# Optimization experiments

Measured on AMD Instinct MI355X. Metric: run time of the kernel, lower is better.

The kernel has to match this reference:

```python
import jax, jax.numpy as jnp
import numpy as np

R1, R2 = 0.1, 0.2  # initial_radius(0.0125) * 8, * 16
EPS = 1e-5

def sqdist(a, b):
    # a [B,N,3], b [B,M,3] -> [B,N,M]
    return jnp.sum(a * a, -1)[:, :, None] + jnp.sum(b * b, -1)[:, None, :] - 2.0 * jnp.einsum('bnc,bmc->bnm', a, b)

def gather(p, idx):
    # p [B,N,C], idx [B,...] -> [B,...,C]
    return jax.vmap(lambda pp, ii: pp[ii])(p, idx)

def fps(xyz, npoint):
    # farthest point sampling, returns int32 [B,npoint]
    B, N, _ = xyz.shape
    def step(carry, _):
        dist, far = carry
        cen = xyz[jnp.arange(B), far]                       # [B,3]
        d = jnp.sum((xyz - cen[:, None, :]) ** 2, -1)       # [B,N]
        dist = jnp.minimum(dist, d)
        nxt = jnp.argmax(dist, -1).astype(jnp.int32)
        return (dist, nxt), far
    init = (jnp.full((B, N), 1e10, xyz.dtype), jnp.zeros(B, jnp.int32))
    _, idx = jax.lax.scan(step, init, None, length=npoint)
    return idx.T

def ball_query(xyz, new_xyz, radius, nsample):
    d = sqdist(new_xyz, xyz)                                # [B,S,N]
    N = xyz.shape[1]
    cand = jnp.where(d <= radius * radius, jnp.arange(N, dtype=jnp.int32), jnp.int32(N))
    idx = -jax.lax.top_k(-cand, nsample)[0]                 # smallest nsample in-ball indices
    first = idx[..., :1]
    idx = jnp.where(idx == N, first, idx)                   # pad with first neighbor
    nearest = jnp.argmin(d, -1, keepdims=True).astype(jnp.int32)
    return jnp.where(idx == N, nearest, idx)                # fallback if ball empty

def bn_relu(x, g, b, axes):
    # training-mode batchnorm (biased var) + relu, channel-last
    m = jnp.mean(x, axes, keepdims=True)
    v = jnp.mean((x - m) ** 2, axes, keepdims=True)
    return jax.nn.relu((x - m) * jax.lax.rsqrt(v + EPS) * g + b)

def set_abstraction(xyz, feat, npoint, radius, nsample, layers):
    new_xyz = gather(xyz, fps(xyz, npoint))                 # [B,S,3]
    gidx = ball_query(xyz, new_xyz, radius, nsample)        # [B,S,K]
    gx = gather(xyz, gidx) - new_xyz[:, :, None, :]         # [B,S,K,3]
    h = jnp.concatenate([gx, gather(feat, gidx)], -1)       # [B,S,K,3+C]
    for w, g, b in layers:
        h = bn_relu(jnp.einsum('bskc,oc->bsko', h, w), g, b, (0, 1, 2))
    return new_xyz, jnp.max(h, 2)                           # [B,S,Cout]

def set_upconv(pos1, pos2, feat1, feat2, nsample, w1, g1, b1, w2, g2, b2):
    idx = jax.lax.top_k(-sqdist(pos1, pos2), nsample)[1]    # knn into sparse cloud [B,N,K]
    gp = gather(pos2, idx) - pos1[:, :, None, :]
    h = jnp.concatenate([gather(feat2, idx), gp], -1)       # [B,N,K,C2+3]
    h = bn_relu(jnp.einsum('bnkc,oc->bnko', h, w1), g1, b1, (0, 1, 2))
    h = jnp.max(h, 2)
    h = jnp.concatenate([h, feat1], -1)                     # [B,N,mlp[-1]+C1]
    return bn_relu(jnp.einsum('bnc,oc->bno', h, w2), g2, b2, (0, 1))

def feature_prop(pos1, pos2, feat1, feat2, w, g, b):
    negd, idx = jax.lax.top_k(-sqdist(pos1, pos2), 3)       # 3-NN
    dist = jnp.maximum(-negd, 1e-10)
    wgt = 1.0 / dist
    wgt = wgt / jnp.sum(wgt, -1, keepdims=True)
    interp = jnp.sum(gather(feat2, idx) * wgt[..., None], 2)
    h = jnp.concatenate([interp, feat1], -1)
    return bn_relu(jnp.einsum('bnc,oc->bno', h, w), g, b, (0, 1))

def _forward(points1, fea1, points2, fea2,
             sa1_w0, sa1_g0, sa1_b0, sa1_w1, sa1_g1, sa1_b1,
             sa2_w0, sa2_g0, sa2_b0, sa2_w1, sa2_g1, sa2_b1,
             su1_w1, su1_g1, su1_b1, su1_w2, su1_g2, su1_b2,
             fp_w, fp_g, fp_b, bn1_g, bn1_b, conv2_w, conv2_b):
    def pipeline(pts, fea):
        l1x, l1f = set_abstraction(pts, fea, 4096, R1, 16,
                                   [(sa1_w0, sa1_g0, sa1_b0), (sa1_w1, sa1_g1, sa1_b1)])
        l2x, l2f = set_abstraction(l1x, l1f, 1024, R2, 16,
                                   [(sa2_w0, sa2_g0, sa2_b0), (sa2_w1, sa2_g1, sa2_b1)])
        l1n = set_upconv(l1x, l2x, l1f, l2f, 8, su1_w1, su1_g1, su1_b1, su1_w2, su1_g2, su1_b2)
        l0n = feature_prop(pts, l1x, fea, l1n, fp_w, fp_g, fp_b)
        x = bn_relu(l0n, bn1_g, bn1_b, (0, 1))              # relu(bn1(.))
        sf = jnp.einsum('bnc,oc->bno', x, conv2_w) + conv2_b
        return jnp.concatenate([pts, sf], -1)               # include_pos
    return jnp.stack([pipeline(points1, fea1), pipeline(points2, fea2)])  # [2,B,N,19]

def setup_inputs() -> dict:
    key = jax.random.key(0)
    ks = jax.random.split(key, 12)
    B, N, C = 2, 8192, 10
    def w(k, o, i):
        return jax.random.normal(k, (o, i), jnp.float32) * 0.1
    inp = {
        'points1': jax.random.uniform(ks[0], (B, N, 3), jnp.float32),
        'fea1': jax.random.normal(ks[1], (B, N, C), jnp.float32),
        'points2': jax.random.uniform(ks[2], (B, N, 3), jnp.float32),
        'fea2': jax.random.normal(ks[3], (B, N, C), jnp.float32),
        'sa1_w0': w(ks[4], 16, 13), 'sa1_g0': jnp.ones(16), 'sa1_b0': jnp.zeros(16),
        'sa1_w1': w(ks[5], 32, 16), 'sa1_g1': jnp.ones(32), 'sa1_b1': jnp.zeros(32),
        'sa2_w0': w(ks[6], 32, 35), 'sa2_g0': jnp.ones(32), 'sa2_b0': jnp.zeros(32),
        'sa2_w1': w(ks[7], 64, 32), 'sa2_g1': jnp.ones(64), 'sa2_b1': jnp.zeros(64),
        'su1_w1': w(ks[8], 32, 67), 'su1_g1': jnp.ones(32), 'su1_b1': jnp.zeros(32),
        'su1_w2': w(ks[9], 32, 64), 'su1_g2': jnp.ones(32), 'su1_b2': jnp.zeros(32),
        'fp_w': w(ks[10], 32, 42), 'fp_g': jnp.ones(32), 'fp_b': jnp.zeros(32),
        'bn1_g': jnp.ones(32), 'bn1_b': jnp.zeros(32),
        'conv2_w': w(ks[11], 16, 32), 'conv2_b': jnp.zeros(16),
    }
    return inp

def reference(points1, fea1, points2, fea2,
              sa1_w0, sa1_g0, sa1_b0, sa1_w1, sa1_g1, sa1_b1,
              sa2_w0, sa2_g0, sa2_b0, sa2_w1, sa2_g1, sa2_b1,
              su1_w1, su1_g1, su1_b1, su1_w2, su1_g2, su1_b2,
              fp_w, fp_g, fp_b, bn1_g, bn1_b, conv2_w, conv2_b):
    return _forward(points1, fea1, points2, fea2,
                    sa1_w0, sa1_g0, sa1_b0, sa1_w1, sa1_g1, sa1_b1,
                    sa2_w0, sa2_g0, sa2_b0, sa2_w1, sa2_g1, sa2_b1,
                    su1_w1, su1_g1, su1_b1, su1_w2, su1_g2, su1_b2,
                    fp_w, fp_g, fp_b, bn1_g, bn1_b, conv2_w, conv2_b)
```

## Files before the change

### kernel.cpp

```cpp
#include <hip/hip_runtime.h>

#define DI __device__ __forceinline__

enum : int {
  OFF_XYZF = 0,
  OFF_FEAF = OFF_XYZF + 4*8192*3,
  OFF_NX1  = OFF_FEAF + 4*8192*10,
  OFF_L1F  = OFF_NX1  + 4*4096*3,
  OFF_NX2  = OFF_L1F  + 4*4096*32,
  OFF_L2F  = OFF_NX2  + 4*1024*3,
  OFF_UH2  = OFF_L2F  + 4*1024*64,
  OFF_L1N  = OFF_UH2  + 4*4096*32,
  OFF_H3   = OFF_L1N  + 4*4096*32,
  OFF_L0N  = OFF_H3   + 4*8192*32,
  OFF_STATS= OFF_L0N  + 4*8192*32,
  OFF_GIDX1= OFF_STATS + 2048,
  OFF_GIDX2= OFF_GIDX1 + 4*4096*16,
  OFF_UIDX = OFF_GIDX2 + 4*1024*16,
  WS_END   = OFF_UIDX + 4*4096*8
};
enum : int { ST_SA1A=0, ST_SA1B=64, ST_SA2A=128, ST_SA2B=192, ST_U1=320, ST_U2=384, ST_FP=448, ST_BN1=512 };

DI float nrm3(float x, float y, float z){ return fmaf(z,z, fmaf(y,y, x*x)); }
DI float dot3(float ax,float ay,float az,float bx,float by,float bz){
  return fmaf(az,bz, fmaf(ay,by, ax*bx));
}

template<int CTRL>
DI double kstage(double v){
  int lo = __builtin_amdgcn_update_dpp(0, __double2loint(v), CTRL, 0xf, 0xf, true);
  int hi = __builtin_amdgcn_update_dpp(0, __double2hiint(v), CTRL, 0xf, 0xf, true);
  return fmax(v, __hiloint2double(hi, lo));
}
DI double red63_kmax(double v){
  v = kstage<0x111>(v);
  v = kstage<0x112>(v);
  v = kstage<0x114>(v);
  v = kstage<0x118>(v);
  v = kstage<0x142>(v);
  v = kstage<0x143>(v);
  return v;
}

template<int CH>
DI void stats_accum(float* h, float* dst, float (*sred)[128])
{
  float sq[CH];
  #pragma unroll
  for (int c=0;c<CH;c++) sq[c]=h[c]*h[c];
  #pragma unroll
  for (int m=1;m<64;m<<=1){
    #pragma unroll
    for (int c=0;c<CH;c++){ h[c] += __shfl_xor(h[c], m, 64); sq[c] += __shfl_xor(sq[c], m, 64); }
  }
  const int tid=threadIdx.x, wid=tid>>6, lane=tid&63;
  if (lane==0){
    #pragma unroll
    for (int c=0;c<CH;c++){ sred[wid][c]=h[c]; sred[wid][CH+c]=sq[c]; }
  }
  __syncthreads();
  if (tid < 2*CH){
    float v = sred[0][tid]+sred[1][tid]+sred[2][tid]+sred[3][tid];
    atomicAdd(dst+tid, v);
  }
}

__global__ __launch_bounds__(256) void prep(const float* __restrict__ p1,const float* __restrict__ f1,
                                            const float* __restrict__ p2,const float* __restrict__ f2,
                                            float* __restrict__ xyzf, float* __restrict__ feaf)
{
  const int i = blockIdx.x*256+threadIdx.x;
  const int z = i>>13, n = i&8191, pipe=z>>1, b=z&1;
  const float* ps = (pipe?p2:p1) + (b*8192+n)*3;
  const float* fs = (pipe?f2:f1) + (b*8192+n)*10;
  float* xo = xyzf + (z*8192+n)*3;
  float* fo = feaf + (z*8192+n)*10;
  #pragma unroll
  for (int c=0;c<3;c++)  xo[c]=ps[c];
  #pragma unroll
  for (int c=0;c<10;c++) fo[c]=fs[c];
}

template<int N,int NPOINT,int T>
__global__ __launch_bounds__(T) void fps_kernel(const float* __restrict__ src, float* __restrict__ dst)
{
  constexpr int P = N/T;
  const int z = blockIdx.x;
  const float* xyz = src + z*N*3;
  float* nx = dst + z*NPOINT*3;
  const int t = threadIdx.x;
  __shared__ float sx[N], sy[N], szz[N];
  __shared__ int swin[NPOINT];
  __shared__ unsigned long long s_acc[3];
  float px[P],py[P],pz[P],dist[P];
  #pragma unroll
  for (int k=0;k<P;k++){
    const int j = t + k*T;
    float x=xyz[j*3+0], y=xyz[j*3+1], w=xyz[j*3+2];
    px[k]=x; py[k]=y; pz[k]=w; dist[k]=1e10f;
    sx[j]=x; sy[j]=y; szz[j]=w;
  }
  if (t==0){ s_acc[0]=0ull; s_acc[1]=0ull; s_acc[2]=0ull; }
  __syncthreads();
  unsigned long long win = (unsigned long long)(unsigned)(N-1);
  for (int s=0;;s++){
    const int cur = (N-1) - (int)(unsigned)(win & 0xffffffffull);
    if (t==0) swin[s] = cur;
    if (s == NPOINT-1) break;
    const float cx=sx[cur], cy=sy[cur], cz=szz[cur];
    float lm = -1.0f;
    #pragma unroll
    for (int k=0;k<P;k+=2){
      float dx0=px[k]-cx,   dy0=py[k]-cy,   dz0=pz[k]-cz;
      float dx1=px[k+1]-cx, dy1=py[k+1]-cy, dz1=pz[k+1]-cz;
      float d0 = fmaf(dz0,dz0, fmaf(dy0,dy0, dx0*dx0));
      float d1 = fmaf(dz1,dz1, fmaf(dy1,dy1, dx1*dx1));
      float n0 = fminf(dist[k],   d0);
      float n1 = fminf(dist[k+1], d1);
      dist[k]=n0; dist[k+1]=n1;
      lm = fmaxf(lm, fmaxf(n0,n1));
    }
    int kb = 0;
    #pragma unroll
    for (int k=P-1;k>=0;k--) if (dist[k]==lm) kb = k;
    double mykey = __hiloint2double(__float_as_int(lm), N-1 - (t + kb*T));
    double wk = red63_kmax(mykey);
    if ((t&63)==63)
      atomicMax(&s_acc[s%3], (unsigned long long)__double_as_longlong(wk));
    if (t==0) s_acc[(s+1)%3] = 0ull;
    __syncthreads();
    win = s_acc[s%3];
  }
  __syncthreads();
  for (int i=t;i<NPOINT;i+=T){
    int j = swin[i];
    nx[i*3]=sx[j]; nx[i*3+1]=sy[j]; nx[i*3+2]=szz[j];
  }
}

template<int NSRC,int SQ,int K>
__global__ __launch_bounds__(64) void ball_query(const float* __restrict__ qxyz, const float* __restrict__ sxyz,
                                                 int* __restrict__ gidx, float r2)
{
  __shared__ float4 tile[1024];
  const int z = blockIdx.y, tid = threadIdx.x;
  const int s = blockIdx.x*64 + tid;
  const float* q = qxyz + (z*SQ+s)*3;
  const float qx=q[0],qy=q[1],qz=q[2];
  const float qq=nrm3(qx,qy,qz);
  int cnt=0, first=0, amin=0; float dmin=3.0e38f;
  int* out = gidx + (z*SQ+s)*K;
  for (int t0=0;t0<NSRC;t0+=1024){
    __syncthreads();
    for (int i=tid;i<1024;i+=64){
      const float* p = sxyz + (z*NSRC+t0+i)*3;
      float x=p[0],y=p[1],w=p[2];
      tile[i]=make_float4(x,y,w,nrm3(x,y,w));
    }
    __syncthreads();
    for (int jj=0;jj<1024;jj++){
      float4 p = tile[jj];
      float dot=dot3(qx,qy,qz,p.x,p.y,p.z);
      float d=(qq+p.w)-2.0f*dot;
      const int j = t0+jj;
      if (d < dmin){ dmin=d; amin=j; }
      if (d <= r2 && cnt < K){ if(cnt==0) first=j; out[cnt]=j; cnt++; }
    }
  }
  const int fill = (cnt==0)? amin : first;
  for (int c=cnt;c<K;c++) out[c]=fill;
}

template<int S,int K,int CF,int C1,int C2,int NSRC,int PASS>
__global__ __launch_bounds__(256) void sa_pass(
    const float* __restrict__ srcxyz, const float* __restrict__ srcfea,
    const float* __restrict__ qxyz, const int* __restrict__ gidx,
    const float* __restrict__ w0, const float* __restrict__ g0, const float* __restrict__ b0,
    const float* __restrict__ w1, const float* __restrict__ g1v, const float* __restrict__ b1v,
    float* __restrict__ stats, int offA, int offB, float cnt0, float cnt1,
    float* __restrict__ outp)
{
  constexpr int CIN = 3+CF;
  __shared__ float w0l[C1*CIN];
  __shared__ float w1l[PASS>=2 ? C2*C1 : 1];
  __shared__ float sc0[C1], bi0[C1];
  __shared__ float sc1[C2], bi1[C2];
  __shared__ float sred[4][128];
  const int z = blockIdx.y, pipe = z>>1, tid = threadIdx.x;
  float* stA = stats + pipe*1024 + offA;
  float* stB = stats + pipe*1024 + offB;
  for (int i=tid;i<C1*CIN;i+=256) w0l[i]=w0[i];
  if (PASS>=2){
    for (int i=tid;i<C2*C1;i+=256) w1l[i]=w1[i];
    if (tid<C1){
      float m = stA[tid]/cnt0;
      float var = stA[C1+tid]/cnt0 - m*m;
      float rs = 1.0f/sqrtf(var+1e-5f);
      float sc = rs*g0[tid];
      sc0[tid]=sc; bi0[tid]=b0[tid]-m*sc;
    }
  }
  if (PASS==3 && tid<C2){
    float m = stB[tid]/cnt1;
    float var = stB[C2+tid]/cnt1 - m*m;
    float rs = 1.0f/sqrtf(var+1e-5f);
    float sc = rs*g1v[tid];
    sc1[tid]=sc; bi1[tid]=b1v[tid]-m*sc;
  }
  __syncthreads();
  const int item = blockIdx.x*256+tid;
  const int s = item/K;
  const int j = gidx[(z*S+s)*K + (item%K)];
  const float* q = qxyz + (z*S+s)*3;
  const float* p = srcxyz + (z*NSRC+j)*3;
  float f[CIN];
  f[0]=p[0]-q[0]; f[1]=p[1]-q[1]; f[2]=p[2]-q[2];
  const float* fe = srcfea + (z*NSRC+j)*CF;
  #pragma unroll
  for (int c=0;c<CF;c++) f[3+c]=fe[c];
  float h1[C1];
  #pragma unroll
  for (int o=0;o<C1;o++){
    float a=0.f;
    #pragma unroll
    for (int c=0;c<CIN;c++) a = fmaf(w0l[o*CIN+c], f[c], a);
    h1[o]=a;
  }
  if (PASS==1){ stats_accum<C1>(h1, stA, sred); return; }
  float f2v[C1];
  #pragma unroll
  for (int o=0;o<C1;o++) f2v[o]=fmaxf(fmaf(h1[o],sc0[o],bi0[o]), 0.f);
  float h2[C2];
  #pragma unroll
  for (int o=0;o<C2;o++){
    float a=0.f;
    #pragma unroll
    for (int c=0;c<C1;c++) a = fmaf(w1l[o*C1+c], f2v[c], a);
    h2[o]=a;
  }
  if (PASS==2){ stats_accum<C2>(h2, stB, sred); return; }
  #pragma unroll
  for (int o=0;o<C2;o++) h2[o]=fmaxf(fmaf(h2[o],sc1[o],bi1[o]), 0.f);
  #pragma unroll
  for (int msk=1; msk<K; msk<<=1){
    #pragma unroll
    for (int o=0;o<C2;o++) h2[o]=fmaxf(h2[o], __shfl_xor(h2[o], msk, 64));
  }
  if ((tid & (K-1))==0){
    float* op = outp + (z*S+s)*C2;
    #pragma unroll
    for (int o=0;o<C2;o++) op[o]=h2[o];
  }
}

__global__ __launch_bounds__(64) void up_top8(const float* __restrict__ nx1, const float* __restrict__ nx2,
                                              int* __restrict__ uidx)
{
  __shared__ float4 tile[1024];
  const int z=blockIdx.y, tid=threadIdx.x;
  const int s=blockIdx.x*64+tid;
  const float* q = nx1 + (z*4096+s)*3;
  const float qx=q[0],qy=q[1],qz=q[2];
  const float qq=nrm3(qx,qy,qz);
  for (int i=tid;i<1024;i+=64){
    const float* p = nx2 + (z*1024+i)*3;
    float x=p[0],y=p[1],w=p[2];
    tile[i]=make_float4(x,y,w,nrm3(x,y,w));
  }
  __syncthreads();
  float d[8]; int id[8];
  #pragma unroll
  for (int r=0;r<8;r++){ d[r]=3e38f; id[r]=0; }
  for (int j=0;j<1024;j++){
    float4 p=tile[j];
    float dt=dot3(qx,qy,qz,p.x,p.y,p.z);
    float dd=(qq+p.w)-2.0f*dt;
    if (dd<d[7]){
      d[7]=dd; id[7]=j;
      #pragma unroll
      for (int r=7;r>0;r--){
        if (d[r]<d[r-1]){ float td=d[r-1]; d[r-1]=d[r]; d[r]=td; int ti=id[r-1]; id[r-1]=id[r]; id[r]=ti; }
      }
    }
  }
  int* o = uidx + (z*4096+s)*8;
  #pragma unroll
  for (int r=0;r<8;r++) o[r]=id[r];
}

template<int PASS>
__global__ __launch_bounds__(256) void up_pass(
    const float* __restrict__ nx1, const float* __restrict__ nx2,
    const float* __restrict__ l2f, const float* __restrict__ l1f,
    const int* __restrict__ uidx,
    const float* __restrict__ w1, const float* __restrict__ g1v, const float* __restrict__ b1v,
    const float* __restrict__ w2,
    float* __restrict__ stats, float* __restrict__ uh2)
{
  __shared__ float w1l[32*67];
  __shared__ float w2l[PASS==2?32*64:1];
  __shared__ float sc0[32], bi0[32];
  __shared__ float sred[4][128];
  const int z=blockIdx.y, pipe=z>>1, tid=threadIdx.x;
  float* stU1 = stats + pipe*1024 + ST_U1;
  float* stU2 = stats + pipe*1024 + ST_U2;
  for (int i=tid;i<32*67;i+=256) w1l[i]=w1[i];
  if (PASS==2){
    for (int i=tid;i<32*64;i+=256) w2l[i]=w2[i];
    if (tid<32){
      float m=stU1[tid]/65536.f;
      float var=stU1[32+tid]/65536.f - m*m;
      float rs=1.0f/sqrtf(var+1e-5f);
      float sc=rs*g1v[tid];
      sc0[tid]=sc; bi0[tid]=b1v[tid]-m*sc;
    }
  }
  __syncthreads();
  const int item = blockIdx.x*256+tid;
  const int s = item>>3, k = item&7;
  const int j = uidx[(z*4096+s)*8+k];
  float f67[67];
  const float* fe = l2f + (z*1024+j)*64;
  #pragma unroll
  for (int c=0;c<64;c++) f67[c]=fe[c];
  const float* pp = nx2 + (z*1024+j)*3;
  const float* qv = nx1 + (z*4096+s)*3;
  f67[64]=pp[0]-qv[0]; f67[65]=pp[1]-qv[1]; f67[66]=pp[2]-qv[2];
  float h[32];
  #pragma unroll
  for (int o=0;o<32;o++){
    float a=0.f;
    #pragma unroll
    for (int c=0;c<67;c++) a=fmaf(w1l[o*67+c], f67[c], a);
    h[o]=a;
  }
  if (PASS==1){ stats_accum<32>(h, stU1, sred); return; }
  #pragma unroll
  for (int o=0;o<32;o++) h[o]=fmaxf(fmaf(h[o],sc0[o],bi0[o]),0.f);
  #pragma unroll
  for (int msk=1; msk<8; msk<<=1){
    #pragma unroll
    for (int o=0;o<32;o++) h[o]=fmaxf(h[o], __shfl_xor(h[o],msk,64));
  }
  float h2[32];
  if (k==0){
    const float* l1 = l1f + (z*4096+s)*32;
    #pragma unroll
    for (int o=0;o<32;o++){
      float a=0.f;
      #pragma unroll
      for (int c=0;c<32;c++) a=fmaf(w2l[o*64+c], h[c], a);
      #pragma unroll
      for (int c=0;c<32;c++) a=fmaf(w2l[o*64+32+c], l1[c], a);
      h2[o]=a;
    }
    float* up = uh2 + (z*4096+s)*32;
    #pragma unroll
    for (int o=0;o<32;o++) up[o]=h2[o];
  } else {
    #pragma unroll
    for (int o=0;o<32;o++) h2[o]=0.f;
  }
  stats_accum<32>(h2, stU2, sred);
}

__global__ __launch_bounds__(256) void up_norm(const float* __restrict__ uh2, const float* __restrict__ g,
                                               const float* __restrict__ b, const float* __restrict__ stats,
                                               float* __restrict__ l1n)
{
  const int i = blockIdx.x*256+threadIdx.x;
  const int z = i>>17, pipe = z>>1, c = i&31;
  const float* st = stats + pipe*1024 + ST_U2;
  float m = st[c]/8192.f;
  float var = st[32+c]/8192.f - m*m;
  float rs = 1.0f/sqrtf(var+1e-5f);
  float sc = rs*g[c];
  float bi = b[c]-m*sc;
  l1n[i]=fmaxf(fmaf(uh2[i],sc,bi),0.f);
}

__global__ __launch_bounds__(256) void fp_kern(
  const float* __restrict__ xyzf, const float* __restrict__ feaf,
  const float* __restrict__ nx1, const float* __restrict__ l1n,
  const float* __restrict__ fpw, float* __restrict__ stats, float* __restrict__ h3)
{
  __shared__ float4 tile[2048];
  __shared__ float wl[32*42];
  __shared__ float sred[4][128];
  const int z=blockIdx.y, pipe=z>>1, tid=threadIdx.x;
  for (int i=tid;i<32*42;i+=256) wl[i]=fpw[i];
  const int n = blockIdx.x*256+tid;
  const float* q = xyzf + (z*8192+n)*3;
  const float qx=q[0],qy=q[1],qz=q[2];
  const float qq2=nrm3(qx,qy,qz);
  float d0=3e38f,d1=3e38f,d2=3e38f; int i0=0,i1=0,i2=0;
  for (int t0=0;t0<4096;t0+=2048){
    __syncthreads();
    for (int i=tid;i<2048;i+=256){
      const float* p = nx1 + (z*4096+t0+i)*3;
      float x=p[0],y=p[1],w=p[2];
      tile[i]=make_float4(x,y,w,nrm3(x,y,w));
    }
    __syncthreads();
    for (int jj=0;jj<2048;jj++){
      float4 p=tile[jj];
      float dt=dot3(qx,qy,qz,p.x,p.y,p.z);
      float d=(qq2+p.w)-2.0f*dt;
      if (d<d2){
        d2=d; i2=t0+jj;
        if (d2<d1){ float td=d1; d1=d2; d2=td; int ti=i1; i1=i2; i2=ti; }
        if (d1<d0){ float td=d0; d0=d1; d1=td; int ti=i0; i0=i1; i1=ti; }
      }
    }
  }
  d0=fmaxf(d0,1e-10f); d1=fmaxf(d1,1e-10f); d2=fmaxf(d2,1e-10f);
  float w0=1.0f/d0, w1=1.0f/d1, w2=1.0f/d2;
  float wsum=(w0+w1)+w2;
  w0/=wsum; w1/=wsum; w2/=wsum;
  const float* A = l1n + (z*4096+i0)*32;
  const float* B = l1n + (z*4096+i1)*32;
  const float* C = l1n + (z*4096+i2)*32;
  float f[42];
  #pragma unroll
  for (int c=0;c<32;c++) f[c]=fmaf(C[c],w2, fmaf(B[c],w1, A[c]*w0));
  const float* fe = feaf + (z*8192+n)*10;
  #pragma unroll
  for (int c=0;c<10;c++) f[32+c]=fe[c];
  float h[32];
  #pragma unroll
  for (int o=0;o<32;o++){
    float a=0.f;
    #pragma unroll
    for (int c=0;c<42;c++) a=fmaf(wl[o*42+c], f[c], a);
    h[o]=a;
    h3[(z*8192+n)*32+o]=a;
  }
  stats_accum<32>(h, stats + pipe*1024 + ST_FP, sred);
}

__global__ __launch_bounds__(256) void fp_post(const float* __restrict__ h3, const float* __restrict__ g,
                                               const float* __restrict__ b, float* __restrict__ stats,
                                               float* __restrict__ l0n)
{
  __shared__ float sc[32], bi[32];
  __shared__ float sred[4][128];
  const int tid=threadIdx.x;
  const int row = blockIdx.x*256+tid;
  const int pipe = row>>14;
  float* stF = stats + pipe*1024 + ST_FP;
  float* stB = stats + pipe*1024 + ST_BN1;
  if (tid<32){
    float m=stF[tid]/16384.f;
    float var=stF[32+tid]/16384.f-m*m;
    float rs=1.0f/sqrtf(var+1e-5f);
    float s=rs*g[tid];
    sc[tid]=s; bi[tid]=b[tid]-m*s;
  }
  __syncthreads();
  float x[32];
  #pragma unroll
  for (int c=0;c<32;c++){ x[c]=fmaxf(fmaf(h3[row*32+c],sc[c],bi[c]),0.f); l0n[row*32+c]=x[c]; }
  stats_accum<32>(x, stB, sred);
}

__global__ __launch_bounds__(256) void final_kern(
  const float* __restrict__ l0n, const float* __restrict__ g, const float* __restrict__ b,
  const float* __restrict__ cw, const float* __restrict__ cb,
  const float* __restrict__ p1, const float* __restrict__ p2,
  const float* __restrict__ stats, float* __restrict__ out)
{
  __shared__ float sc[32], bi[32], wl[512], bl[16];
  const int tid=threadIdx.x;
  const int row = blockIdx.x*256+tid;
  const int z=row>>13, pipe=z>>1, bb=z&1, n=row&8191;
  const float* st = stats + pipe*1024 + ST_BN1;
  if (tid<32){
    float m=st[tid]/16384.f;
    float var=st[32+tid]/16384.f-m*m;
    float rs=1.0f/sqrtf(var+1e-5f);
    float s=rs*g[tid];
    sc[tid]=s; bi[tid]=b[tid]-m*s;
  }
  for (int i=tid;i<512;i+=256) wl[i]=cw[i];
  if (tid<16) bl[tid]=cb[tid];
  __syncthreads();
  float x[32];
  #pragma unroll
  for (int c=0;c<32;c++) x[c]=fmaxf(fmaf(l0n[row*32+c],sc[c],bi[c]),0.f);
  float* o = out + row*19;
  const float* ps = (pipe?p2:p1) + (bb*8192+n)*3;
  o[0]=ps[0]; o[1]=ps[1]; o[2]=ps[2];
  #pragma unroll
  for (int oo=0;oo<16;oo++){
    float a=0.f;
    #pragma unroll
    for (int c=0;c<32;c++) a=fmaf(wl[oo*32+c],x[c],a);
    o[3+oo]=a+bl[oo];
  }
}

extern "C" void kernel_launch(void* const* d_in, const int* in_sizes, int n_in,
                              void* d_out, int out_size, void* d_ws, size_t ws_size,
                              hipStream_t stream)
{
  (void)in_sizes; (void)n_in; (void)out_size; (void)ws_size;
  const float* p1 = (const float*)d_in[0];
  const float* f1 = (const float*)d_in[1];
  const float* p2 = (const float*)d_in[2];
  const float* f2 = (const float*)d_in[3];
  const float *sa1_w0=(const float*)d_in[4], *sa1_g0=(const float*)d_in[5], *sa1_b0=(const float*)d_in[6];
  const float *sa1_w1=(const float*)d_in[7], *sa1_g1=(const float*)d_in[8], *sa1_b1=(const float*)d_in[9];
  const float *sa2_w0=(const float*)d_in[10],*sa2_g0=(const float*)d_in[11],*sa2_b0=(const float*)d_in[12];
  const float *sa2_w1=(const float*)d_in[13],*sa2_g1=(const float*)d_in[14],*sa2_b1=(const float*)d_in[15];
  const float *su1_w1=(const float*)d_in[16],*su1_g1=(const float*)d_in[17],*su1_b1=(const float*)d_in[18];
  const float *su1_w2=(const float*)d_in[19],*su1_g2=(const float*)d_in[20],*su1_b2=(const float*)d_in[21];
  const float *fp_w=(const float*)d_in[22], *fp_g=(const float*)d_in[23], *fp_b=(const float*)d_in[24];
  const float *bn1_g=(const float*)d_in[25],*bn1_b=(const float*)d_in[26];
  const float *conv2_w=(const float*)d_in[27],*conv2_b=(const float*)d_in[28];
  float* wsf=(float*)d_ws; int* wsi=(int*)d_ws;
  float* xyzf=wsf+OFF_XYZF; float* feaf=wsf+OFF_FEAF;
  float* nx1=wsf+OFF_NX1; float* l1f=wsf+OFF_L1F;
  float* nx2=wsf+OFF_NX2; float* l2f=wsf+OFF_L2F;
  float* uh2=wsf+OFF_UH2; float* l1n=wsf+OFF_L1N;
  float* h3=wsf+OFF_H3; float* l0n=wsf+OFF_L0N;
  float* stats=wsf+OFF_STATS;
  int* gidx1=wsi+OFF_GIDX1; int* gidx2=wsi+OFF_GIDX2; int* uidx=wsi+OFF_UIDX;
  const float R2A=(float)(0.1*0.1), R2B=(float)(0.2*0.2);

  (void)hipMemsetAsync(stats, 0, 2048*sizeof(float), stream);
  prep<<<128,256,0,stream>>>(p1,f1,p2,f2,xyzf,feaf);
  fps_kernel<8192,4096,512><<<4,512,0,stream>>>(xyzf, nx1);
  ball_query<8192,4096,16><<<dim3(64,4),64,0,stream>>>(nx1, xyzf, gidx1, R2A);
  sa_pass<4096,16,10,16,32,8192,1><<<dim3(256,4),256,0,stream>>>(xyzf,feaf,nx1,gidx1,
      sa1_w0,sa1_g0,sa1_b0,sa1_w1,sa1_g1,sa1_b1, stats,ST_SA1A,ST_SA1B,131072.f,131072.f, l1f);
  sa_pass<4096,16,10,16,32,8192,2><<<dim3(256,4),256,0,stream>>>(xyzf,feaf,nx1,gidx1,
      sa1_w0,sa1_g0,sa1_b0,sa1_w1,sa1_g1,sa1_b1, stats,ST_SA1A,ST_SA1B,131072.f,131072.f, l1f);
  sa_pass<4096,16,10,16,32,8192,3><<<dim3(256,4),256,0,stream>>>(xyzf,feaf,nx1,gidx1,
      sa1_w0,sa1_g0,sa1_b0,sa1_w1,sa1_g1,sa1_b1, stats,ST_SA1A,ST_SA1B,131072.f,131072.f, l1f);
  fps_kernel<4096,1024,512><<<4,512,0,stream>>>(nx1, nx2);
  ball_query<4096,1024,16><<<dim3(16,4),64,0,stream>>>(nx2, nx1, gidx2, R2B);
  sa_pass<1024,16,32,32,64,4096,1><<<dim3(64,4),256,0,stream>>>(nx1,l1f,nx2,gidx2,
      sa2_w0,sa2_g0,sa2_b0,sa2_w1,sa2_g1,sa2_b1, stats,ST_SA2A,ST_SA2B,32768.f,32768.f, l2f);
  sa_pass<1024,16,32,32,64,4096,2><<<dim3(64,4),256,0,stream>>>(nx1,l1f,nx2,gidx2,
      sa2_w0,sa2_g0,sa2_b0,sa2_w1,sa2_g1,sa2_b1, stats,ST_SA2A,ST_SA2B,32768.f,32768.f, l2f);
  sa_pass<1024,16,32,32,64,4096,3><<<dim3(64,4),256,0,stream>>>(nx1,l1f,nx2,gidx2,
      sa2_w0,sa2_g0,sa2_b0,sa2_w1,sa2_g1,sa2_b1, stats,ST_SA2A,ST_SA2B,32768.f,32768.f, l2f);
  up_top8<<<dim3(64,4),64,0,stream>>>(nx1,nx2,uidx);
  up_pass<1><<<dim3(128,4),256,0,stream>>>(nx1,nx2,l2f,l1f,uidx,su1_w1,su1_g1,su1_b1,su1_w2,stats,uh2);
  up_pass<2><<<dim3(128,4),256,0,stream>>>(nx1,nx2,l2f,l1f,uidx,su1_w1,su1_g1,su1_b1,su1_w2,stats,uh2);
  up_norm<<<2048,256,0,stream>>>(uh2,su1_g2,su1_b2,stats,l1n);
  fp_kern<<<dim3(32,4),256,0,stream>>>(xyzf,feaf,nx1,l1n,fp_w,stats,h3);
  fp_post<<<128,256,0,stream>>>(h3,fp_g,fp_b,stats,l0n);
  final_kern<<<128,256,0,stream>>>(l0n,bn1_g,bn1_b,conv2_w,conv2_b,p1,p2,stats,(float*)d_out);
}
```

Before: 5.482 ms.

## Pack FPS distance math into float2 vectors and enlarge query kernel blocks

The FPS inner loop now holds point coordinates and running distances as two-wide float vectors, so the compiler can emit packed FP32 FMA/min/max instructions. Ball query and up_top8 move from 64-thread to 256-thread blocks, which cuts the grid fourfold. This is meant to reduce redundant tile staging per query, at the cost of fewer blocks, only 64 or 16 workgroups on a large GPU. Unroll pragmas are also added to the distance scan loops in ball query, up_top8 and the FP kernel.

```diff
diff --git a/kernel.cpp b/kernel.cpp
--- a/kernel.cpp
+++ b/kernel.cpp
@@ -1,6 +1,8 @@
 #include <hip/hip_runtime.h>
 
 #define DI __device__ __forceinline__
+
+typedef float f32x2 __attribute__((ext_vector_type(2)));
 
 enum : int {
   OFF_XYZF = 0,
@@ -84,7 +86,7 @@
 template<int N,int NPOINT,int T>
 __global__ __launch_bounds__(T) void fps_kernel(const float* __restrict__ src, float* __restrict__ dst)
 {
-  constexpr int P = N/T;
+  constexpr int P = N/T, H = P/2;
   const int z = blockIdx.x;
   const float* xyz = src + z*N*3;
   float* nx = dst + z*NPOINT*3;
@@ -92,13 +94,16 @@
   __shared__ float sx[N], sy[N], szz[N];
   __shared__ int swin[NPOINT];
   __shared__ unsigned long long s_acc[3];
-  float px[P],py[P],pz[P],dist[P];
-  #pragma unroll
-  for (int k=0;k<P;k++){
-    const int j = t + k*T;
-    float x=xyz[j*3+0], y=xyz[j*3+1], w=xyz[j*3+2];
-    px[k]=x; py[k]=y; pz[k]=w; dist[k]=1e10f;
-    sx[j]=x; sy[j]=y; szz[j]=w;
+  f32x2 px2[H],py2[H],pz2[H],dist2[H];
+  #pragma unroll
+  for (int i=0;i<H;i++){
+    const int j0 = t + (2*i)*T, j1 = t + (2*i+1)*T;
+    float x0=xyz[j0*3+0], y0=xyz[j0*3+1], w0=xyz[j0*3+2];
+    float x1=xyz[j1*3+0], y1=xyz[j1*3+1], w1=xyz[j1*3+2];
+    px2[i]=(f32x2){x0,x1}; py2[i]=(f32x2){y0,y1}; pz2[i]=(f32x2){w0,w1};
+    dist2[i]=(f32x2){1e10f,1e10f};
+    sx[j0]=x0; sy[j0]=y0; szz[j0]=w0;
+    sx[j1]=x1; sy[j1]=y1; szz[j1]=w1;
   }
   if (t==0){ s_acc[0]=0ull; s_acc[1]=0ull; s_acc[2]=0ull; }
   __syncthreads();
@@ -108,21 +113,23 @@
     if (t==0) swin[s] = cur;
     if (s == NPOINT-1) break;
     const float cx=sx[cur], cy=sy[cur], cz=szz[cur];
-    float lm = -1.0f;
-    #pragma unroll
-    for (int k=0;k<P;k+=2){
-      float dx0=px[k]-cx,   dy0=py[k]-cy,   dz0=pz[k]-cz;
-      float dx1=px[k+1]-cx, dy1=py[k+1]-cy, dz1=pz[k+1]-cz;
-      float d0 = fmaf(dz0,dz0, fmaf(dy0,dy0, dx0*dx0));
-      float d1 = fmaf(dz1,dz1, fmaf(dy1,dy1, dx1*dx1));
-      float n0 = fminf(dist[k],   d0);
-      float n1 = fminf(dist[k+1], d1);
-      dist[k]=n0; dist[k+1]=n1;
-      lm = fmaxf(lm, fmaxf(n0,n1));
-    }
+    const f32x2 cx2=(f32x2){cx,cx}, cy2=(f32x2){cy,cy}, cz2=(f32x2){cz,cz};
+    f32x2 lm2=(f32x2){-1.f,-1.f};
+    #pragma unroll
+    for (int i=0;i<H;i++){
+      f32x2 dx = px2[i]-cx2, dy = py2[i]-cy2, dz = pz2[i]-cz2;
+      f32x2 d  = __builtin_elementwise_fma(dz,dz, __builtin_elementwise_fma(dy,dy, dx*dx));
+      f32x2 nd = __builtin_elementwise_min(dist2[i], d);
+      dist2[i] = nd;
+      lm2 = __builtin_elementwise_max(lm2, nd);
+    }
+    const float lm = fmaxf(lm2.x, lm2.y);
     int kb = 0;
     #pragma unroll
-    for (int k=P-1;k>=0;k--) if (dist[k]==lm) kb = k;
+    for (int k=P-1;k>=0;k--){
+      float dk = (k&1) ? dist2[k>>1].y : dist2[k>>1].x;
+      if (dk==lm) kb = k;
+    }
     double mykey = __hiloint2double(__float_as_int(lm), N-1 - (t + kb*T));
     double wk = red63_kmax(mykey);
     if ((t&63)==63)
@@ -139,12 +146,12 @@
 }
 
 template<int NSRC,int SQ,int K>
-__global__ __launch_bounds__(64) void ball_query(const float* __restrict__ qxyz, const float* __restrict__ sxyz,
-                                                 int* __restrict__ gidx, float r2)
+__global__ __launch_bounds__(256) void ball_query(const float* __restrict__ qxyz, const float* __restrict__ sxyz,
+                                                  int* __restrict__ gidx, float r2)
 {
   __shared__ float4 tile[1024];
   const int z = blockIdx.y, tid = threadIdx.x;
-  const int s = blockIdx.x*64 + tid;
+  const int s = blockIdx.x*256 + tid;
   const float* q = qxyz + (z*SQ+s)*3;
   const float qx=q[0],qy=q[1],qz=q[2];
   const float qq=nrm3(qx,qy,qz);
@@ -152,12 +159,13 @@
   int* out = gidx + (z*SQ+s)*K;
   for (int t0=0;t0<NSRC;t0+=1024){
     __syncthreads();
-    for (int i=tid;i<1024;i+=64){
+    for (int i=tid;i<1024;i+=256){
       const float* p = sxyz + (z*NSRC+t0+i)*3;
       float x=p[0],y=p[1],w=p[2];
       tile[i]=make_float4(x,y,w,nrm3(x,y,w));
     }
     __syncthreads();
+    #pragma unroll 4
     for (int jj=0;jj<1024;jj++){
       float4 p = tile[jj];
       float dot=dot3(qx,qy,qz,p.x,p.y,p.z);
@@ -253,16 +261,16 @@
   }
 }
 
-__global__ __launch_bounds__(64) void up_top8(const float* __restrict__ nx1, const float* __restrict__ nx2,
-                                              int* __restrict__ uidx)
+__global__ __launch_bounds__(256) void up_top8(const float* __restrict__ nx1, const float* __restrict__ nx2,
+                                               int* __restrict__ uidx)
 {
   __shared__ float4 tile[1024];
   const int z=blockIdx.y, tid=threadIdx.x;
-  const int s=blockIdx.x*64+tid;
+  const int s=blockIdx.x*256+tid;
   const float* q = nx1 + (z*4096+s)*3;
   const float qx=q[0],qy=q[1],qz=q[2];
   const float qq=nrm3(qx,qy,qz);
-  for (int i=tid;i<1024;i+=64){
+  for (int i=tid;i<1024;i+=256){
     const float* p = nx2 + (z*1024+i)*3;
     float x=p[0],y=p[1],w=p[2];
     tile[i]=make_float4(x,y,w,nrm3(x,y,w));
@@ -271,6 +279,7 @@
   float d[8]; int id[8];
   #pragma unroll
   for (int r=0;r<8;r++){ d[r]=3e38f; id[r]=0; }
+  #pragma unroll 4
   for (int j=0;j<1024;j++){
     float4 p=tile[j];
     float dt=dot3(qx,qy,qz,p.x,p.y,p.z);
@@ -402,6 +411,7 @@
       tile[i]=make_float4(x,y,w,nrm3(x,y,w));
     }
     __syncthreads();
+    #pragma unroll 2
     for (int jj=0;jj<2048;jj++){
       float4 p=tile[jj];
       float dt=dot3(qx,qy,qz,p.x,p.y,p.z);
@@ -530,7 +540,7 @@
   (void)hipMemsetAsync(stats, 0, 2048*sizeof(float), stream);
   prep<<<128,256,0,stream>>>(p1,f1,p2,f2,xyzf,feaf);
   fps_kernel<8192,4096,512><<<4,512,0,stream>>>(xyzf, nx1);
-  ball_query<8192,4096,16><<<dim3(64,4),64,0,stream>>>(nx1, xyzf, gidx1, R2A);
+  ball_query<8192,4096,16><<<dim3(16,4),256,0,stream>>>(nx1, xyzf, gidx1, R2A);
   sa_pass<4096,16,10,16,32,8192,1><<<dim3(256,4),256,0,stream>>>(xyzf,feaf,nx1,gidx1,
       sa1_w0,sa1_g0,sa1_b0,sa1_w1,sa1_g1,sa1_b1, stats,ST_SA1A,ST_SA1B,131072.f,131072.f, l1f);
   sa_pass<4096,16,10,16,32,8192,2><<<dim3(256,4),256,0,stream>>>(xyzf,feaf,nx1,gidx1,
@@ -538,14 +548,14 @@
   sa_pass<4096,16,10,16,32,8192,3><<<dim3(256,4),256,0,stream>>>(xyzf,feaf,nx1,gidx1,
       sa1_w0,sa1_g0,sa1_b0,sa1_w1,sa1_g1,sa1_b1, stats,ST_SA1A,ST_SA1B,131072.f,131072.f, l1f);
   fps_kernel<4096,1024,512><<<4,512,0,stream>>>(nx1, nx2);
-  ball_query<4096,1024,16><<<dim3(16,4),64,0,stream>>>(nx2, nx1, gidx2, R2B);
+  ball_query<4096,1024,16><<<dim3(4,4),256,0,stream>>>(nx2, nx1, gidx2, R2B);
   sa_pass<1024,16,32,32,64,4096,1><<<dim3(64,4),256,0,stream>>>(nx1,l1f,nx2,gidx2,
       sa2_w0,sa2_g0,sa2_b0,sa2_w1,sa2_g1,sa2_b1, stats,ST_SA2A,ST_SA2B,32768.f,32768.f, l2f);
   sa_pass<1024,16,32,32,64,4096,2><<<dim3(64,4),256,0,stream>>>(nx1,l1f,nx2,gidx2,
       sa2_w0,sa2_g0,sa2_b0,sa2_w1,sa2_g1,sa2_b1, stats,ST_SA2A,ST_SA2B,32768.f,32768.f, l2f);
   sa_pass<1024,16,32,32,64,4096,3><<<dim3(64,4),256,0,stream>>>(nx1,l1f,nx2,gidx2,
       sa2_w0,sa2_g0,sa2_b0,sa2_w1,sa2_g1,sa2_b1, stats,ST_SA2A,ST_SA2B,32768.f,32768.f, l2f);
-  up_top8<<<dim3(64,4),64,0,stream>>>(nx1,nx2,uidx);
+  up_top8<<<dim3(16,4),256,0,stream>>>(nx1,nx2,uidx);
   up_pass<1><<<dim3(128,4),256,0,stream>>>(nx1,nx2,l2f,l1f,uidx,su1_w1,su1_g1,su1_b1,su1_w2,stats,uh2);
   up_pass<2><<<dim3(128,4),256,0,stream>>>(nx1,nx2,l2f,l1f,uidx,su1_w1,su1_g1,su1_b1,su1_w2,stats,uh2);
   up_norm<<<2048,256,0,stream>>>(uh2,su1_g2,su1_b2,stats,l1n);
```

New measurement: 5.913 ms. +7.9%, slower.
